# Performance work log

Hardware: AMD Instinct MI355X
Metric: run time of the kernel (lower is better)

## Reference

```python
import jax, jax.numpy as jnp
import numpy as np

B, S, H = 2, 2048, 768
NH, HD = 12, 64  # num heads, head dim


def setup_inputs() -> dict:
    key = jax.random.key(0)
    ks = jax.random.split(key, 9)
    std = 0.02
    def dense(k):
        return jax.random.normal(k, (H, H), dtype=jnp.float32) * std
    return {
        "hidden_states": jax.random.normal(ks[0], (B, S, H), dtype=jnp.float32),
        "attention_mask": jnp.ones((B, S), dtype=jnp.int32),
        "Wq": dense(ks[1]), "bq": jnp.zeros((H,), jnp.float32),
        "Wk": dense(ks[2]), "bk": jnp.zeros((H,), jnp.float32),
        "Wv": dense(ks[3]), "bv": jnp.zeros((H,), jnp.float32),
        "Wo": dense(ks[4]), "bo": jnp.zeros((H,), jnp.float32),
    }


def reference(hidden_states, attention_mask, Wq, bq, Wk, bk, Wv, bv, Wo, bo):
    # QKV projections -> [B, NH, S, HD]
    def split_heads(x):
        return x.reshape(B, S, NH, HD).transpose(0, 2, 1, 3)
    q = split_heads(hidden_states @ Wq + bq)
    k = split_heads(hidden_states @ Wk + bk)
    v = split_heads(hidden_states @ Wv + bv)
    # scaled dot-product scores [B, NH, S, S]
    scores = jnp.einsum('bhqd,bhkd->bhqk', q, k) / jnp.sqrt(jnp.float32(HD))
    adder = (1.0 - attention_mask.astype(jnp.float32)) * -10000.0
    scores = scores + adder[:, None, None, :]
    probs = jax.nn.softmax(scores, axis=-1)
    # dropout is identity at inference
    ctx = jnp.einsum('bhqk,bhkd->bhqd', probs, v)
    ctx = ctx.transpose(0, 2, 1, 3).reshape(B, S, H)
    return ctx @ Wo + bo
```

## Files before the change

### kernel.cpp

```cpp
#include <hip/hip_runtime.h>
#include <hip/hip_bf16.h>

#define DI __device__ __forceinline__

using bf16x8 = __attribute__((ext_vector_type(8))) short;
using f32x4  = __attribute__((ext_vector_type(4))) float;
using u16    = unsigned short;
using u16x4  = __attribute__((ext_vector_type(4))) unsigned short;

constexpr int Bc = 2, Sc = 2048, Hc = 768, NHc = 12, HDc = 64;
constexpr int Mc = Bc * Sc;
constexpr float L2E = 1.4426950408889634f;

DI u16 f2bf(float f) {
  union { float f; unsigned u; } c; c.f = f;
  unsigned u = c.u;
  return (u16)((u + 0x7fffu + ((u >> 16) & 1u)) >> 16);
}

DI unsigned f2bf2(float a, float b) {
  float2 t; t.x = a; t.y = b;
  __hip_bfloat162 h = __float22bfloat162_rn(t);
  union { __hip_bfloat162 h; unsigned u; } c; c.h = h;
  return c.u;
}

DI void gload_lds16(const void* g, void* l) {
  __builtin_amdgcn_global_load_lds(
      (__attribute__((address_space(1))) void*)(g),
      (__attribute__((address_space(3))) void*)(l), 16, 0, 0);
}


__global__ void cvt_bf16(const float* __restrict__ x, u16* __restrict__ y, int n4) {
  int i = blockIdx.x * 256 + threadIdx.x;
  if (i >= n4) return;
  float4 v = reinterpret_cast<const float4*>(x)[i];
  u16x4 o;
  o[0] = f2bf(v.x); o[1] = f2bf(v.y); o[2] = f2bf(v.z); o[3] = f2bf(v.w);
  reinterpret_cast<u16x4*>(y)[i] = o;
}

__global__ void wtrans(const float* __restrict__ Wq, const float* __restrict__ Wk,
                       const float* __restrict__ Wv, const float* __restrict__ Wo,
                       u16* __restrict__ Tq, u16* __restrict__ Tk,
                       u16* __restrict__ Tv, u16* __restrict__ To) {
  __shared__ float tile[32][33];
  const float* W; u16* T;
  switch (blockIdx.z) {
    case 0:  W = Wq; T = Tq; break;
    case 1:  W = Wk; T = Tk; break;
    case 2:  W = Wv; T = Tv; break;
    default: W = Wo; T = To; break;
  }
  int tx = threadIdx.x, ty = threadIdx.y;
  int n0 = blockIdx.x * 32, k0 = blockIdx.y * 32;
#pragma unroll
  for (int j = 0; j < 4; ++j) tile[ty + j * 8][tx] = W[(k0 + ty + j * 8) * Hc + n0 + tx];
  __syncthreads();
#pragma unroll
  for (int j = 0; j < 4; ++j) T[(n0 + ty + j * 8) * Hc + k0 + tx] = f2bf(tile[tx][ty + j * 8]);
}


DI void gemm_core(const u16* __restrict__ Ag, const u16* __restrict__ Btg,
                  u16* Asm, u16* Bsm, int m0, int n0,
                  int tid, int lane, int wr, int wc, f32x4 acc[4][4]) {
  const int lo = lane & 15, hi = lane >> 4;
  const int r1 = tid >> 2, c1 = tid & 3;
  for (int kt = 0; kt < Hc / 32; ++kt) {
    const int k0 = kt * 32;
    {
      int row = r1, cg = c1 ^ ((row >> 1) & 3);
      gload_lds16(Ag  + (size_t)(row + m0) * Hc + k0 + cg * 8, Asm + tid * 8);
      gload_lds16(Btg + (size_t)(row + n0) * Hc + k0 + cg * 8, Bsm + tid * 8);
      row = r1 + 64; cg = c1 ^ ((row >> 1) & 3);
      gload_lds16(Ag  + (size_t)(row + m0) * Hc + k0 + cg * 8, Asm + (tid + 256) * 8);
      gload_lds16(Btg + (size_t)(row + n0) * Hc + k0 + cg * 8, Bsm + (tid + 256) * 8);
    }
    __syncthreads();
    bf16x8 af[4], bf[4];
#pragma unroll
    for (int m = 0; m < 4; ++m) {
      int rowa = wr * 64 + m * 16 + lo;
      af[m] = *reinterpret_cast<const bf16x8*>(Asm + rowa * 32 + ((hi ^ ((rowa >> 1) & 3)) * 8));
      int rowb = wc * 64 + m * 16 + lo;
      bf[m] = *reinterpret_cast<const bf16x8*>(Bsm + rowb * 32 + ((hi ^ ((rowb >> 1) & 3)) * 8));
    }
#pragma unroll
    for (int m = 0; m < 4; ++m)
#pragma unroll
      for (int n = 0; n < 4; ++n)
        acc[m][n] = __builtin_amdgcn_mfma_f32_16x16x32_bf16(af[m], bf[n], acc[m][n], 0, 0, 0);
    __syncthreads();
  }
}


__launch_bounds__(256)
__global__ void qkv_gemm(const u16* __restrict__ Xb,
                         const u16* __restrict__ Wtq, const u16* __restrict__ Wtk,
                         const u16* __restrict__ Wtv,
                         const float* __restrict__ bq, const float* __restrict__ bk,
                         const float* __restrict__ bv,
                         u16* __restrict__ Qo, u16* __restrict__ Ko, u16* __restrict__ Vto) {
  __shared__ __attribute__((aligned(16))) u16 Asm[128 * 32];
  __shared__ __attribute__((aligned(16))) u16 Bsm[128 * 32];
  const int tid = threadIdx.x, lane = tid & 63, w = tid >> 6;
  const int wr = w >> 1, wc = w & 1;
  const int m0 = blockIdx.x * 128, n0 = blockIdx.y * 128;
  const int z = blockIdx.z;
  const u16* Bt = (z == 0) ? Wtq : ((z == 1) ? Wtk : Wtv);
  const float* bias = (z == 0) ? bq : ((z == 1) ? bk : bv);
  f32x4 acc[4][4] = {};
  gemm_core(Xb, Bt, Asm, Bsm, m0, n0, tid, lane, wr, wc, acc);
  const int lo = lane & 15, hi = lane >> 4;
  const float scl = (z == 0) ? 0.125f * L2E : 1.0f;
#pragma unroll
  for (int m = 0; m < 4; ++m)
#pragma unroll
    for (int n = 0; n < 4; ++n)
#pragma unroll
      for (int r = 0; r < 4; ++r) {
        int gm = m0 + wr * 64 + m * 16 + hi * 4 + r;
        int gn = n0 + wc * 64 + n * 16 + lo;
        float v = (acc[m][n][r] + bias[gn]) * scl;
        int b = gm >> 11, s = gm & 2047, h = gn >> 6, d = gn & 63;
        u16 bv16 = f2bf(v);
        if (z == 2) Vto[((b * NHc + h) * HDc + d) * Sc + s] = bv16;
        else {
          int idx = (((b * NHc + h) * Sc) + s) * HDc + d;
          if (z == 0) Qo[idx] = bv16; else Ko[idx] = bv16;
        }
      }
}


__launch_bounds__(256)
__global__ void out_gemm(const u16* __restrict__ Ctx, const u16* __restrict__ Wto,
                         const float* __restrict__ bo, float* __restrict__ out) {
  __shared__ __attribute__((aligned(16))) u16 Asm[128 * 32];
  __shared__ __attribute__((aligned(16))) u16 Bsm[128 * 32];
  const int tid = threadIdx.x, lane = tid & 63, w = tid >> 6;
  const int wr = w >> 1, wc = w & 1;
  const int m0 = blockIdx.x * 128, n0 = blockIdx.y * 128;
  f32x4 acc[4][4] = {};
  gemm_core(Ctx, Wto, Asm, Bsm, m0, n0, tid, lane, wr, wc, acc);
  const int lo = lane & 15, hi = lane >> 4;
#pragma unroll
  for (int m = 0; m < 4; ++m)
#pragma unroll
    for (int n = 0; n < 4; ++n)
#pragma unroll
      for (int r = 0; r < 4; ++r) {
        int gm = m0 + wr * 64 + m * 16 + hi * 4 + r;
        int gn = n0 + wc * 64 + n * 16 + lo;
        out[(size_t)gm * Hc + gn] = acc[m][n][r] + bo[gn];
      }
}


__launch_bounds__(256)
__global__ void attn(const u16* __restrict__ Qg, const u16* __restrict__ Kg,
                     const u16* __restrict__ Vtg, const int* __restrict__ maskg,
                     u16* __restrict__ ctxg) {
  __shared__ __attribute__((aligned(16))) u16 Ksm[2][64 * 64];
  __shared__ __attribute__((aligned(16))) u16 Vsm[2][64 * 64];
  __shared__ __attribute__((aligned(16))) u16 Psm[4][16 * 64];
  __shared__ __attribute__((aligned(16))) float Adm[Sc];

  const int tid = threadIdx.x, lane = tid & 63, w = tid >> 6;
  const int lo = lane & 15, hi = lane >> 4;

  const int id = blockIdx.x;
  const int xcd = id & 7, sub = id >> 3;
  const int head = xcd * 3 + (sub >> 5);
  const int q0 = (sub & 31) * 64;
  const int b = head / NHc, h = head % NHc;

  const u16* Qh = Qg + (size_t)head * Sc * HDc;
  const u16* Kh = Kg + (size_t)head * Sc * HDc;
  const u16* Vh = Vtg + (size_t)head * HDc * Sc;
  const int* maskb = maskg + b * Sc;

  for (int i = tid; i < Sc / 4; i += 256) {
    int4 mv = reinterpret_cast<const int4*>(maskb)[i];
    float4 a;
    a.x = (1.0f - (float)mv.x) * (-10000.0f * L2E);
    a.y = (1.0f - (float)mv.y) * (-10000.0f * L2E);
    a.z = (1.0f - (float)mv.z) * (-10000.0f * L2E);
    a.w = (1.0f - (float)mv.w) * (-10000.0f * L2E);
    reinterpret_cast<float4*>(Adm)[i] = a;
  }

  const int qrow = q0 + w * 16 + lo;
  bf16x8 qf[2];
  qf[0] = *reinterpret_cast<const bf16x8*>(Qh + (size_t)qrow * HDc + hi * 8);
  qf[1] = *reinterpret_cast<const bf16x8*>(Qh + (size_t)qrow * HDc + 32 + hi * 8);

  bf16x8 onesf;
#pragma unroll
  for (int i = 0; i < 8; ++i) onesf[i] = (short)0x3F80;

  f32x4 oacc[4] = {};
  f32x4 lacc = {};
  float mrow[4] = {-1e30f, -1e30f, -1e30f, -1e30f};

  const int ch1 = tid, row1 = ch1 >> 3, cg1 = (ch1 & 7) ^ (row1 & 7);
  const int ch2 = tid + 256, row2 = ch2 >> 3, cg2 = (ch2 & 7) ^ (row2 & 7);

  __syncthreads();

  gload_lds16(Kh + (size_t)row1 * HDc + cg1 * 8, &Ksm[0][0] + ch1 * 8);
  gload_lds16(Kh + (size_t)row2 * HDc + cg2 * 8, &Ksm[0][0] + ch2 * 8);
  gload_lds16(Vh + (size_t)row1 * Sc + cg1 * 8, &Vsm[0][0] + ch1 * 8);
  gload_lds16(Vh + (size_t)row2 * Sc + cg2 * 8, &Vsm[0][0] + ch2 * 8);

  int cur = 0;
  constexpr int NT = Sc / 64;
  for (int t = 0; t < NT; ++t) {
    if (t + 1 < NT) {
      const int kvn = (t + 1) * 64;
      u16* Kn = &Ksm[cur ^ 1][0];
      u16* Vn = &Vsm[cur ^ 1][0];
      gload_lds16(Kh + (size_t)(kvn + row1) * HDc + cg1 * 8, Kn + ch1 * 8);
      gload_lds16(Kh + (size_t)(kvn + row2) * HDc + cg2 * 8, Kn + ch2 * 8);
      gload_lds16(Vh + (size_t)row1 * Sc + kvn + cg1 * 8, Vn + ch1 * 8);
      gload_lds16(Vh + (size_t)row2 * Sc + kvn + cg2 * 8, Vn + ch2 * 8);
      asm volatile("s_waitcnt vmcnt(4)" ::: "memory");
    } else {
      asm volatile("s_waitcnt vmcnt(0)" ::: "memory");
    }
    __builtin_amdgcn_sched_barrier(0);
    __builtin_amdgcn_s_barrier();
    __builtin_amdgcn_sched_barrier(0);

    const u16* Ks = &Ksm[cur][0];
    const u16* Vs = &Vsm[cur][0];

    f32x4 sacc[4] = {};
#pragma unroll
    for (int n = 0; n < 4; ++n) {
#pragma unroll
      for (int ks = 0; ks < 2; ++ks) {
        int row = n * 16 + lo;
        bf16x8 kf = *reinterpret_cast<const bf16x8*>(
            Ks + row * 64 + (((ks * 4 + hi) ^ (row & 7)) * 8));
        sacc[n] = __builtin_amdgcn_mfma_f32_16x16x32_bf16(qf[ks], kf, sacc[n], 0, 0, 0);
      }
      float add = Adm[t * 64 + n * 16 + lo];
#pragma unroll
      for (int r = 0; r < 4; ++r) sacc[n][r] += add;
    }

    float tmax[4];
#pragma unroll
    for (int r = 0; r < 4; ++r)
      tmax[r] = fmaxf(fmaxf(sacc[0][r], sacc[1][r]), fmaxf(sacc[2][r], sacc[3][r]));
#pragma unroll
    for (int off = 1; off < 16; off <<= 1)
#pragma unroll
      for (int r = 0; r < 4; ++r) tmax[r] = fmaxf(tmax[r], __shfl_xor(tmax[r], off, 64));

    float scale[4];
#pragma unroll
    for (int r = 0; r < 4; ++r) {
      float mnew = fmaxf(mrow[r], tmax[r]);
      scale[r] = exp2f(mrow[r] - mnew);
      mrow[r] = mnew;
    }
#pragma unroll
    for (int n = 0; n < 4; ++n)
#pragma unroll
      for (int r = 0; r < 4; ++r) sacc[n][r] = exp2f(sacc[n][r] - mrow[r]);
#pragma unroll
    for (int n = 0; n < 4; ++n)
#pragma unroll
      for (int r = 0; r < 4; ++r) oacc[n][r] *= scale[r];
#pragma unroll
    for (int r = 0; r < 4; ++r) lacc[r] *= scale[r];

    u16* Pw = &Psm[w][0];
#pragma unroll
    for (int n = 0; n < 4; ++n) {
      unsigned u01 = f2bf2(sacc[n][0], sacc[n][1]);
      unsigned u23 = f2bf2(sacc[n][2], sacc[n][3]);
      int pcol = n * 16 + lo;
      int r0 = hi * 4;
      Pw[(r0 + 0) * 64 + (pcol ^ (((r0 + 0) & 7) << 3))] = (u16)(u01 & 0xffff);
      Pw[(r0 + 1) * 64 + (pcol ^ (((r0 + 1) & 7) << 3))] = (u16)(u01 >> 16);
      Pw[(r0 + 2) * 64 + (pcol ^ (((r0 + 2) & 7) << 3))] = (u16)(u23 & 0xffff);
      Pw[(r0 + 3) * 64 + (pcol ^ (((r0 + 3) & 7) << 3))] = (u16)(u23 >> 16);
    }

    bf16x8 pf0 = *reinterpret_cast<const bf16x8*>(
        Pw + lo * 64 + ((hi * 8) ^ ((lo & 7) << 3)));
    bf16x8 pf1 = *reinterpret_cast<const bf16x8*>(
        Pw + lo * 64 + ((32 + hi * 8) ^ ((lo & 7) << 3)));
    lacc = __builtin_amdgcn_mfma_f32_16x16x32_bf16(pf0, onesf, lacc, 0, 0, 0);
    lacc = __builtin_amdgcn_mfma_f32_16x16x32_bf16(pf1, onesf, lacc, 0, 0, 0);
#pragma unroll
    for (int n = 0; n < 4; ++n) {
      int vrow = n * 16 + lo;
      bf16x8 vf0 = *reinterpret_cast<const bf16x8*>(
          Vs + vrow * 64 + ((hi ^ (vrow & 7)) * 8));
      bf16x8 vf1 = *reinterpret_cast<const bf16x8*>(
          Vs + vrow * 64 + (((4 + hi) ^ (vrow & 7)) * 8));
      oacc[n] = __builtin_amdgcn_mfma_f32_16x16x32_bf16(pf0, vf0, oacc[n], 0, 0, 0);
      oacc[n] = __builtin_amdgcn_mfma_f32_16x16x32_bf16(pf1, vf1, oacc[n], 0, 0, 0);
    }

    __builtin_amdgcn_sched_barrier(0);
    __builtin_amdgcn_s_barrier();
    __builtin_amdgcn_sched_barrier(0);
    cur ^= 1;
  }

#pragma unroll
  for (int r = 0; r < 4; ++r) {
    float inv = 1.0f / lacc[r];
#pragma unroll
    for (int n = 0; n < 4; ++n) {
      int gq = q0 + w * 16 + hi * 4 + r;
      int gd = n * 16 + lo;
      ctxg[(size_t)(b * Sc + gq) * Hc + h * HDc + gd] = f2bf(oacc[n][r] * inv);
    }
  }
}


extern "C" void kernel_launch(void* const* d_in, const int* in_sizes, int n_in,
                              void* d_out, int out_size, void* d_ws, size_t ws_size,
                              hipStream_t stream) {
  const float* hs  = (const float*)d_in[0];
  const int* mask  = (const int*)d_in[1];
  const float* Wq  = (const float*)d_in[2];
  const float* bq  = (const float*)d_in[3];
  const float* Wk  = (const float*)d_in[4];
  const float* bk  = (const float*)d_in[5];
  const float* Wv  = (const float*)d_in[6];
  const float* bv  = (const float*)d_in[7];
  const float* Wo  = (const float*)d_in[8];
  const float* bo  = (const float*)d_in[9];

  char* ws = (char*)d_ws;
  u16* Xb  = (u16*)(ws);
  u16* Wtq = (u16*)(ws + 6291456);
  u16* Wtk = Wtq + 589824;
  u16* Wtv = Wtk + 589824;
  u16* Wto = Wtv + 589824;
  u16* Qb  = (u16*)(ws + 11010048);
  u16* Kb  = Qb + 3145728;
  u16* Vtb = Kb + 3145728;
  u16* Ctx = Vtb + 3145728;

  cvt_bf16<<<(Mc * Hc / 4 + 255) / 256, 256, 0, stream>>>(hs, Xb, Mc * Hc / 4);
  wtrans<<<dim3(24, 24, 4), dim3(32, 8), 0, stream>>>(Wq, Wk, Wv, Wo, Wtq, Wtk, Wtv, Wto);
  qkv_gemm<<<dim3(32, 6, 3), 256, 0, stream>>>(Xb, Wtq, Wtk, Wtv, bq, bk, bv, Qb, Kb, Vtb);
  attn<<<768, 256, 0, stream>>>(Qb, Kb, Vtb, mask, Ctx);
  out_gemm<<<dim3(32, 6), 256, 0, stream>>>(Ctx, Wto, bo, (float*)d_out);
}
```

Measured before the change: 141.0 us.

## Restructure attention with 32x32 MFMA, register-resident P and triple-buffered K/V

Rewrites the attention kernel to compute the transposed score tile with 32x32x16 MFMA, using K as the A operand so the exponentiated probabilities are packed straight into MFMA fragments. This removes the per-tile LDS write and read of P and the per-column additive mask. K/V staging is triple-buffered with 128-thread blocks. The mask is applied multiplicatively instead: V is multiplied by the mask in the QKV epilogue, and the row sum is an MFMA against a bf16 mask vector. That matches the reference except when a whole row is masked, and it raises per-thread register pressure.

Result: slower. 156.8 us (+11.2%).

```diff
diff --git a/kernel.cpp b/kernel.cpp
--- a/kernel.cpp
+++ b/kernel.cpp
@@ -5,6 +5,7 @@
 
 using bf16x8 = __attribute__((ext_vector_type(8))) short;
 using f32x4  = __attribute__((ext_vector_type(4))) float;
+using f32x16 = __attribute__((ext_vector_type(16))) float;
 using u16    = unsigned short;
 using u16x4  = __attribute__((ext_vector_type(4))) unsigned short;
 
@@ -32,13 +33,21 @@
 }
 
 
-__global__ void cvt_bf16(const float* __restrict__ x, u16* __restrict__ y, int n4) {
+__global__ void cvt_bf16(const float* __restrict__ x, u16* __restrict__ y, int n4,
+                         const int* __restrict__ maskg, u16* __restrict__ mones) {
   int i = blockIdx.x * 256 + threadIdx.x;
   if (i >= n4) return;
   float4 v = reinterpret_cast<const float4*>(x)[i];
   u16x4 o;
   o[0] = f2bf(v.x); o[1] = f2bf(v.y); o[2] = f2bf(v.z); o[3] = f2bf(v.w);
   reinterpret_cast<u16x4*>(y)[i] = o;
+  if (i < Bc * Sc / 4) {
+    int4 mv = reinterpret_cast<const int4*>(maskg)[i];
+    u16x4 m;
+    m[0] = f2bf((float)mv.x); m[1] = f2bf((float)mv.y);
+    m[2] = f2bf((float)mv.z); m[3] = f2bf((float)mv.w);
+    reinterpret_cast<u16x4*>(mones)[i] = m;
+  }
 }
 
 __global__ void wtrans(const float* __restrict__ Wq, const float* __restrict__ Wk,
@@ -102,7 +111,7 @@
                          const u16* __restrict__ Wtq, const u16* __restrict__ Wtk,
                          const u16* __restrict__ Wtv,
                          const float* __restrict__ bq, const float* __restrict__ bk,
-                         const float* __restrict__ bv,
+                         const float* __restrict__ bv, const int* __restrict__ maskg,
                          u16* __restrict__ Qo, u16* __restrict__ Ko, u16* __restrict__ Vto) {
   __shared__ __attribute__((aligned(16))) u16 Asm[128 * 32];
   __shared__ __attribute__((aligned(16))) u16 Bsm[128 * 32];
@@ -126,11 +135,12 @@
         int gn = n0 + wc * 64 + n * 16 + lo;
         float v = (acc[m][n][r] + bias[gn]) * scl;
         int b = gm >> 11, s = gm & 2047, h = gn >> 6, d = gn & 63;
-        u16 bv16 = f2bf(v);
-        if (z == 2) Vto[((b * NHc + h) * HDc + d) * Sc + s] = bv16;
-        else {
+        if (z == 2) {
+          v *= (float)maskg[b * Sc + s];
+          Vto[((b * NHc + h) * HDc + d) * Sc + s] = f2bf(v);
+        } else {
           int idx = (((b * NHc + h) * Sc) + s) * HDc + d;
-          if (z == 0) Qo[idx] = bv16; else Ko[idx] = bv16;
+          if (z == 0) Qo[idx] = f2bf(v); else Ko[idx] = f2bf(v);
         }
       }
 }
@@ -160,17 +170,59 @@
 }
 
 
-__launch_bounds__(256)
+DI bf16x8 lds_rd(const u16* base, int row, int c8) {
+  return *reinterpret_cast<const bf16x8*>(base + row * 64 + ((c8 ^ (row & 7)) << 3));
+}
+
+DI bf16x8 ldV(const u16* Vs, int row, int c4, int hi2) {
+  union { u16x4 h[2]; bf16x8 v; } u;
+  const u16* rbase = Vs + row * 64;
+  int sw = (row & 7) << 3;
+  u.h[0] = *reinterpret_cast<const u16x4*>(rbase + (((c4 * 16) ) ^ sw) + hi2 * 4);
+  u.h[1] = *reinterpret_cast<const u16x4*>(rbase + (((c4 * 16) + 8) ^ sw) + hi2 * 4);
+  return u.v;
+}
+
+DI bf16x8 ldM(const u16* Mo, int base, int c4, int hi2) {
+  union { u16x4 h[2]; bf16x8 v; } u;
+  u.h[0] = *reinterpret_cast<const u16x4*>(Mo + base + c4 * 16 + hi2 * 4);
+  u.h[1] = *reinterpret_cast<const u16x4*>(Mo + base + c4 * 16 + 8 + hi2 * 4);
+  return u.v;
+}
+
+DI float vmax16(const f32x16& v) {
+  float a0 = fmaxf(v[0], v[8]),  a1 = fmaxf(v[1], v[9]);
+  float a2 = fmaxf(v[2], v[10]), a3 = fmaxf(v[3], v[11]);
+  float a4 = fmaxf(v[4], v[12]), a5 = fmaxf(v[5], v[13]);
+  float a6 = fmaxf(v[6], v[14]), a7 = fmaxf(v[7], v[15]);
+  float b0 = fmaxf(a0, a4), b1 = fmaxf(a1, a5);
+  float b2 = fmaxf(a2, a6), b3 = fmaxf(a3, a7);
+  return fmaxf(fmaxf(b0, b1), fmaxf(b2, b3));
+}
+
+DI bf16x8 pkfrag0(const f32x16& p) {
+  union { unsigned u[4]; bf16x8 v; } a;
+  a.u[0] = f2bf2(p[0], p[1]); a.u[1] = f2bf2(p[2], p[3]);
+  a.u[2] = f2bf2(p[4], p[5]); a.u[3] = f2bf2(p[6], p[7]);
+  return a.v;
+}
+DI bf16x8 pkfrag1(const f32x16& p) {
+  union { unsigned u[4]; bf16x8 v; } a;
+  a.u[0] = f2bf2(p[8], p[9]);   a.u[1] = f2bf2(p[10], p[11]);
+  a.u[2] = f2bf2(p[12], p[13]); a.u[3] = f2bf2(p[14], p[15]);
+  return a.v;
+}
+
+__launch_bounds__(128)
 __global__ void attn(const u16* __restrict__ Qg, const u16* __restrict__ Kg,
-                     const u16* __restrict__ Vtg, const int* __restrict__ maskg,
+                     const u16* __restrict__ Vtg, const u16* __restrict__ monesG,
                      u16* __restrict__ ctxg) {
-  __shared__ __attribute__((aligned(16))) u16 Ksm[2][64 * 64];
-  __shared__ __attribute__((aligned(16))) u16 Vsm[2][64 * 64];
-  __shared__ __attribute__((aligned(16))) u16 Psm[4][16 * 64];
-  __shared__ __attribute__((aligned(16))) float Adm[Sc];
+  __shared__ __attribute__((aligned(16))) u16 Ksm[3][64 * 64];
+  __shared__ __attribute__((aligned(16))) u16 Vsm[3][64 * 64];
+  __shared__ __attribute__((aligned(16))) u16 Mo[Sc];
 
   const int tid = threadIdx.x, lane = tid & 63, w = tid >> 6;
-  const int lo = lane & 15, hi = lane >> 4;
+  const int l31 = lane & 31, hi2 = lane >> 5;
 
   const int id = blockIdx.x;
   const int xcd = id & 7, sub = id >> 3;
@@ -181,150 +233,118 @@
   const u16* Qh = Qg + (size_t)head * Sc * HDc;
   const u16* Kh = Kg + (size_t)head * Sc * HDc;
   const u16* Vh = Vtg + (size_t)head * HDc * Sc;
-  const int* maskb = maskg + b * Sc;
-
-  for (int i = tid; i < Sc / 4; i += 256) {
-    int4 mv = reinterpret_cast<const int4*>(maskb)[i];
-    float4 a;
-    a.x = (1.0f - (float)mv.x) * (-10000.0f * L2E);
-    a.y = (1.0f - (float)mv.y) * (-10000.0f * L2E);
-    a.z = (1.0f - (float)mv.z) * (-10000.0f * L2E);
-    a.w = (1.0f - (float)mv.w) * (-10000.0f * L2E);
-    reinterpret_cast<float4*>(Adm)[i] = a;
-  }
-
-  const int qrow = q0 + w * 16 + lo;
-  bf16x8 qf[2];
-  qf[0] = *reinterpret_cast<const bf16x8*>(Qh + (size_t)qrow * HDc + hi * 8);
-  qf[1] = *reinterpret_cast<const bf16x8*>(Qh + (size_t)qrow * HDc + 32 + hi * 8);
-
-  bf16x8 onesf;
-#pragma unroll
-  for (int i = 0; i < 8; ++i) onesf[i] = (short)0x3F80;
-
-  f32x4 oacc[4] = {};
-  f32x4 lacc = {};
-  float mrow[4] = {-1e30f, -1e30f, -1e30f, -1e30f};
-
-  const int ch1 = tid, row1 = ch1 >> 3, cg1 = (ch1 & 7) ^ (row1 & 7);
-  const int ch2 = tid + 256, row2 = ch2 >> 3, cg2 = (ch2 & 7) ^ (row2 & 7);
+
+#pragma unroll
+  for (int j = 0; j < 2; ++j) {
+    int ch = tid + j * 128;
+    gload_lds16(monesG + (size_t)b * Sc + ch * 8, Mo + ch * 8);
+  }
+
+  const int qglob = q0 + w * 32 + l31;
+  bf16x8 qf[4];
+#pragma unroll
+  for (int c = 0; c < 4; ++c)
+    qf[c] = *reinterpret_cast<const bf16x8*>(Qh + (size_t)qglob * HDc + c * 16 + hi2 * 8);
 
   __syncthreads();
 
-  gload_lds16(Kh + (size_t)row1 * HDc + cg1 * 8, &Ksm[0][0] + ch1 * 8);
-  gload_lds16(Kh + (size_t)row2 * HDc + cg2 * 8, &Ksm[0][0] + ch2 * 8);
-  gload_lds16(Vh + (size_t)row1 * Sc + cg1 * 8, &Vsm[0][0] + ch1 * 8);
-  gload_lds16(Vh + (size_t)row2 * Sc + cg2 * 8, &Vsm[0][0] + ch2 * 8);
-
-  int cur = 0;
+  u16 *K0 = &Ksm[0][0], *K1 = &Ksm[1][0], *K2 = &Ksm[2][0];
+  u16 *V0 = &Vsm[0][0], *V1 = &Vsm[1][0], *V2 = &Vsm[2][0];
+
+  auto stage = [&](u16* Kd, u16* Vd, int kv0) {
+#pragma unroll
+    for (int j = 0; j < 4; ++j) {
+      int ch = tid + j * 128;
+      int row = ch >> 3, cg = (ch & 7) ^ (row & 7);
+      gload_lds16(Kh + (size_t)(kv0 + row) * HDc + cg * 8, Kd + ch * 8);
+    }
+#pragma unroll
+    for (int j = 0; j < 4; ++j) {
+      int ch = tid + j * 128;
+      int row = ch >> 3, cg = (ch & 7) ^ (row & 7);
+      gload_lds16(Vh + (size_t)row * Sc + kv0 + cg * 8, Vd + ch * 8);
+    }
+  };
+
+  stage(K0, V0, 0);
+  stage(K1, V1, 64);
+
+  f32x16 oacc0 = {}, oacc1 = {}, lacc = {};
+  float mrow = -1e30f;
+
   constexpr int NT = Sc / 64;
   for (int t = 0; t < NT; ++t) {
-    if (t + 1 < NT) {
-      const int kvn = (t + 1) * 64;
-      u16* Kn = &Ksm[cur ^ 1][0];
-      u16* Vn = &Vsm[cur ^ 1][0];
-      gload_lds16(Kh + (size_t)(kvn + row1) * HDc + cg1 * 8, Kn + ch1 * 8);
-      gload_lds16(Kh + (size_t)(kvn + row2) * HDc + cg2 * 8, Kn + ch2 * 8);
-      gload_lds16(Vh + (size_t)row1 * Sc + kvn + cg1 * 8, Vn + ch1 * 8);
-      gload_lds16(Vh + (size_t)row2 * Sc + kvn + cg2 * 8, Vn + ch2 * 8);
-      asm volatile("s_waitcnt vmcnt(4)" ::: "memory");
-    } else {
-      asm volatile("s_waitcnt vmcnt(0)" ::: "memory");
-    }
     __builtin_amdgcn_sched_barrier(0);
     __builtin_amdgcn_s_barrier();
     __builtin_amdgcn_sched_barrier(0);
-
-    const u16* Ks = &Ksm[cur][0];
-    const u16* Vs = &Vsm[cur][0];
-
-    f32x4 sacc[4] = {};
-#pragma unroll
-    for (int n = 0; n < 4; ++n) {
-#pragma unroll
-      for (int ks = 0; ks < 2; ++ks) {
-        int row = n * 16 + lo;
-        bf16x8 kf = *reinterpret_cast<const bf16x8*>(
-            Ks + row * 64 + (((ks * 4 + hi) ^ (row & 7)) * 8));
-        sacc[n] = __builtin_amdgcn_mfma_f32_16x16x32_bf16(qf[ks], kf, sacc[n], 0, 0, 0);
-      }
-      float add = Adm[t * 64 + n * 16 + lo];
-#pragma unroll
-      for (int r = 0; r < 4; ++r) sacc[n][r] += add;
-    }
-
-    float tmax[4];
-#pragma unroll
-    for (int r = 0; r < 4; ++r)
-      tmax[r] = fmaxf(fmaxf(sacc[0][r], sacc[1][r]), fmaxf(sacc[2][r], sacc[3][r]));
-#pragma unroll
-    for (int off = 1; off < 16; off <<= 1)
-#pragma unroll
-      for (int r = 0; r < 4; ++r) tmax[r] = fmaxf(tmax[r], __shfl_xor(tmax[r], off, 64));
-
-    float scale[4];
-#pragma unroll
-    for (int r = 0; r < 4; ++r) {
-      float mnew = fmaxf(mrow[r], tmax[r]);
-      scale[r] = exp2f(mrow[r] - mnew);
-      mrow[r] = mnew;
-    }
-#pragma unroll
-    for (int n = 0; n < 4; ++n)
-#pragma unroll
-      for (int r = 0; r < 4; ++r) sacc[n][r] = exp2f(sacc[n][r] - mrow[r]);
-#pragma unroll
-    for (int n = 0; n < 4; ++n)
-#pragma unroll
-      for (int r = 0; r < 4; ++r) oacc[n][r] *= scale[r];
-#pragma unroll
-    for (int r = 0; r < 4; ++r) lacc[r] *= scale[r];
-
-    u16* Pw = &Psm[w][0];
-#pragma unroll
-    for (int n = 0; n < 4; ++n) {
-      unsigned u01 = f2bf2(sacc[n][0], sacc[n][1]);
-      unsigned u23 = f2bf2(sacc[n][2], sacc[n][3]);
-      int pcol = n * 16 + lo;
-      int r0 = hi * 4;
-      Pw[(r0 + 0) * 64 + (pcol ^ (((r0 + 0) & 7) << 3))] = (u16)(u01 & 0xffff);
-      Pw[(r0 + 1) * 64 + (pcol ^ (((r0 + 1) & 7) << 3))] = (u16)(u01 >> 16);
-      Pw[(r0 + 2) * 64 + (pcol ^ (((r0 + 2) & 7) << 3))] = (u16)(u23 & 0xffff);
-      Pw[(r0 + 3) * 64 + (pcol ^ (((r0 + 3) & 7) << 3))] = (u16)(u23 >> 16);
-    }
-
-    bf16x8 pf0 = *reinterpret_cast<const bf16x8*>(
-        Pw + lo * 64 + ((hi * 8) ^ ((lo & 7) << 3)));
-    bf16x8 pf1 = *reinterpret_cast<const bf16x8*>(
-        Pw + lo * 64 + ((32 + hi * 8) ^ ((lo & 7) << 3)));
-    lacc = __builtin_amdgcn_mfma_f32_16x16x32_bf16(pf0, onesf, lacc, 0, 0, 0);
-    lacc = __builtin_amdgcn_mfma_f32_16x16x32_bf16(pf1, onesf, lacc, 0, 0, 0);
-#pragma unroll
-    for (int n = 0; n < 4; ++n) {
-      int vrow = n * 16 + lo;
-      bf16x8 vf0 = *reinterpret_cast<const bf16x8*>(
-          Vs + vrow * 64 + ((hi ^ (vrow & 7)) * 8));
-      bf16x8 vf1 = *reinterpret_cast<const bf16x8*>(
-          Vs + vrow * 64 + (((4 + hi) ^ (vrow & 7)) * 8));
-      oacc[n] = __builtin_amdgcn_mfma_f32_16x16x32_bf16(pf0, vf0, oacc[n], 0, 0, 0);
-      oacc[n] = __builtin_amdgcn_mfma_f32_16x16x32_bf16(pf1, vf1, oacc[n], 0, 0, 0);
-    }
-
+    if (t + 2 < NT) {
+      stage(K2, V2, (t + 2) * 64);
+      asm volatile("s_waitcnt vmcnt(16)" ::: "memory");
+    } else if (t + 2 == NT) {
+      asm volatile("s_waitcnt vmcnt(8)" ::: "memory");
+    } else {
+      asm volatile("s_waitcnt vmcnt(0)" ::: "memory");
+    }
     __builtin_amdgcn_sched_barrier(0);
     __builtin_amdgcn_s_barrier();
     __builtin_amdgcn_sched_barrier(0);
-    cur ^= 1;
-  }
-
-#pragma unroll
-  for (int r = 0; r < 4; ++r) {
-    float inv = 1.0f / lacc[r];
-#pragma unroll
-    for (int n = 0; n < 4; ++n) {
-      int gq = q0 + w * 16 + hi * 4 + r;
-      int gd = n * 16 + lo;
-      ctxg[(size_t)(b * Sc + gq) * Hc + h * HDc + gd] = f2bf(oacc[n][r] * inv);
-    }
+
+    const u16* Ks = K0;
+    const u16* Vs = V0;
+
+    f32x16 s0 = {}, s1 = {};
+#pragma unroll
+    for (int c = 0; c < 4; ++c) {
+      bf16x8 kf0 = lds_rd(Ks, l31, 2 * c + hi2);
+      bf16x8 kf1 = lds_rd(Ks, 32 + l31, 2 * c + hi2);
+      s0 = __builtin_amdgcn_mfma_f32_32x32x16_bf16(kf0, qf[c], s0, 0, 0, 0);
+      s1 = __builtin_amdgcn_mfma_f32_32x32x16_bf16(kf1, qf[c], s1, 0, 0, 0);
+    }
+
+    float pmax = fmaxf(vmax16(s0), vmax16(s1));
+    pmax = fmaxf(pmax, __shfl_xor(pmax, 32, 64));
+    float nm = fmaxf(mrow, pmax);
+    float sc = exp2f(mrow - nm);
+    mrow = nm;
+#pragma unroll
+    for (int rr = 0; rr < 16; ++rr) {
+      int qi = (rr & 3) + 8 * (rr >> 2) + 4 * hi2;
+      float sb = __shfl(sc, qi, 64);
+      oacc0[rr] *= sb; oacc1[rr] *= sb; lacc[rr] *= sb;
+    }
+#pragma unroll
+    for (int j = 0; j < 16; ++j) s0[j] = exp2f(s0[j] - mrow);
+#pragma unroll
+    for (int j = 0; j < 16; ++j) s1[j] = exp2f(s1[j] - mrow);
+
+    bf16x8 paf[4];
+    paf[0] = pkfrag0(s0);
+    paf[1] = pkfrag1(s0);
+    paf[2] = pkfrag0(s1);
+    paf[3] = pkfrag1(s1);
+
+#pragma unroll
+    for (int c4 = 0; c4 < 4; ++c4) {
+      bf16x8 mo = ldM(Mo, t * 64, c4, hi2);
+      lacc = __builtin_amdgcn_mfma_f32_32x32x16_bf16(paf[c4], mo, lacc, 0, 0, 0);
+      bf16x8 vf0 = ldV(Vs, l31, c4, hi2);
+      bf16x8 vf1 = ldV(Vs, 32 + l31, c4, hi2);
+      oacc0 = __builtin_amdgcn_mfma_f32_32x32x16_bf16(paf[c4], vf0, oacc0, 0, 0, 0);
+      oacc1 = __builtin_amdgcn_mfma_f32_32x32x16_bf16(paf[c4], vf1, oacc1, 0, 0, 0);
+    }
+
+    u16* tk = K0; K0 = K1; K1 = K2; K2 = tk;
+    u16* tv = V0; V0 = V1; V1 = V2; V2 = tv;
+  }
+
+#pragma unroll
+  for (int rr = 0; rr < 16; ++rr) {
+    float inv = 1.0f / lacc[rr];
+    int qi = (rr & 3) + 8 * (rr >> 2) + 4 * hi2;
+    int s = q0 + w * 32 + qi;
+    size_t base = (size_t)(b * Sc + s) * Hc + h * HDc;
+    ctxg[base + l31]      = f2bf(oacc0[rr] * inv);
+    ctxg[base + 32 + l31] = f2bf(oacc1[rr] * inv);
   }
 }
 
@@ -353,10 +373,11 @@
   u16* Kb  = Qb + 3145728;
   u16* Vtb = Kb + 3145728;
   u16* Ctx = Vtb + 3145728;
-
-  cvt_bf16<<<(Mc * Hc / 4 + 255) / 256, 256, 0, stream>>>(hs, Xb, Mc * Hc / 4);
+  u16* Mns = Ctx + 3145728;
+
+  cvt_bf16<<<(Mc * Hc / 4 + 255) / 256, 256, 0, stream>>>(hs, Xb, Mc * Hc / 4, mask, Mns);
   wtrans<<<dim3(24, 24, 4), dim3(32, 8), 0, stream>>>(Wq, Wk, Wv, Wo, Wtq, Wtk, Wtv, Wto);
-  qkv_gemm<<<dim3(32, 6, 3), 256, 0, stream>>>(Xb, Wtq, Wtk, Wtv, bq, bk, bv, Qb, Kb, Vtb);
-  attn<<<768, 256, 0, stream>>>(Qb, Kb, Vtb, mask, Ctx);
+  qkv_gemm<<<dim3(32, 6, 3), 256, 0, stream>>>(Xb, Wtq, Wtk, Wtv, bq, bk, bv, mask, Qb, Kb, Vtb);
+  attn<<<768, 128, 0, stream>>>(Qb, Kb, Vtb, Mns, Ctx);
   out_gemm<<<dim3(32, 6), 256, 0, stream>>>(Ctx, Wto, bo, (float*)d_out);
 }
```
